# Performance work log

Measured on AMD Instinct MI355X. Metric: run time of the kernel, lower is better.

## Reference

```python
import jax, jax.numpy as jnp
import numpy as np

EMB = 128
N_TEXT = 80000
N_NODES = 100000
E = 800000
N_REL = 500
PRED_IN = 4 * EMB + 2 * 2 + 2 * 2 * (2 + 2)  # 532


def scatter_mean(x, src, dst, num_nodes):
    # PyG MessagePassing(aggr='mean'): mean of x[src] grouped by dst; empty groups -> 0
    sums = jax.ops.segment_sum(x[src], dst, num_segments=num_nodes)
    cnt = jax.ops.segment_sum(jnp.ones((src.shape[0], 1), x.dtype), dst, num_segments=num_nodes)
    return sums / jnp.maximum(cnt, 1.0)


def setup_inputs() -> dict:
    key = jax.random.key(0)
    ks = jax.random.split(key, 12)
    inp = {
        "h_id_tensor": jax.random.randint(ks[0], (E,), 0, N_NODES),
        "r_id_tensor": jax.random.randint(ks[1], (E,), 0, N_REL),
        "t_id_tensor": jax.random.randint(ks[2], (E,), 0, N_NODES),
        "q_emb": jax.random.normal(ks[3], (1, EMB), jnp.float32),
        "entity_embs": jax.random.normal(ks[4], (N_TEXT, EMB), jnp.float32),
        "num_non_text_entities": N_NODES - N_TEXT,
        "relation_embs": jax.random.normal(ks[5], (N_REL, EMB), jnp.float32),
        "topic_entity_one_hot": jax.random.uniform(ks[6], (N_NODES, 2), jnp.float32),
        # learned params
        "non_text_emb": jax.random.normal(ks[7], (1, EMB), jnp.float32) * 0.02,
        "W1": jax.random.normal(ks[8], (EMB, PRED_IN), jnp.float32) / np.sqrt(PRED_IN),
        "b1": jnp.zeros((EMB,), jnp.float32),
        "W2": jax.random.normal(ks[9], (1, EMB), jnp.float32) / np.sqrt(EMB),
        "b2": jnp.zeros((1,), jnp.float32),
    }
    return inp


def reference(h_id_tensor, r_id_tensor, t_id_tensor, q_emb, entity_embs,
              num_non_text_entities, relation_embs, topic_entity_one_hot,
              non_text_emb, W1, b1, W2, b2):
    num_nodes = entity_embs.shape[0] + num_non_text_entities
    # node embeddings: text entities + shared non-text embedding row
    h_e = jnp.concatenate(
        [entity_embs, jnp.broadcast_to(non_text_emb, (num_non_text_entities, EMB))], axis=0)

    # DDE: forward rounds over (h->t), reverse rounds over (t->h); scatter-mean diffusion
    dde_list = []
    h_pe = topic_entity_one_hot
    for _ in range(2):
        h_pe = scatter_mean(h_pe, h_id_tensor, t_id_tensor, num_nodes)
        dde_list.append(h_pe)
    h_pe_rev = topic_entity_one_hot
    for _ in range(2):
        h_pe_rev = scatter_mean(h_pe_rev, t_id_tensor, h_id_tensor, num_nodes)
        dde_list.append(h_pe_rev)

    h_e_full = jnp.concatenate([h_e, topic_entity_one_hot] + dde_list, axis=1)  # [N, EMB+10]

    h_r = relation_embs[r_id_tensor]                       # [E, EMB]
    h_q = jnp.broadcast_to(q_emb, (h_r.shape[0], EMB))     # [E, EMB]
    h_triple = jnp.concatenate(
        [h_q, h_e_full[h_id_tensor], h_r, h_e_full[t_id_tensor]], axis=1)  # [E, PRED_IN]

    hidden = jax.nn.relu(h_triple @ W1.T + b1)             # [E, EMB]
    pred = hidden @ W2.T + b2                              # [E, 1]
    return pred
```

## Files before the change

### kernel.cpp

```cpp
#include <hip/hip_runtime.h>

#define EMB 128
#define W1LD 532
#define KP 160
#define ST 264
#define BSH 8
#define BNODES 256
#define EPB 4096

typedef unsigned long long u64;
typedef unsigned int u32;
typedef unsigned short u16;
typedef __attribute__((ext_vector_type(8))) short short8;
typedef __attribute__((ext_vector_type(4))) float f32x4;
typedef _Float16 h2 __attribute__((ext_vector_type(2)));

__device__ __forceinline__ u16 f2bf(float x) {
    unsigned u = __float_as_uint(x);
    unsigned r = (u + 0x7fffu + ((u >> 16) & 1u)) >> 16;
    return (u16)r;
}
__device__ __forceinline__ u16 f2h(float x) {
    union { _Float16 h; u16 u; } c; c.h = (_Float16)x; return c.u;
}
__device__ __forceinline__ h2 u2h(unsigned u) {
    union { unsigned u; h2 h; } c; c.u = u; return c.h;
}

__device__ __forceinline__ float ep8(const uint4& ua, const uint4& ub,
                                     const uint4& ur, const uint4& uw, float s) {
    const h2 z = {(_Float16)0.0f, (_Float16)0.0f};
#if __has_builtin(__builtin_amdgcn_fdot2)
#define FDOT2(x, w, s) __builtin_amdgcn_fdot2(x, w, s, false)
#else
#define FDOT2(x, w, s) (s + (float)x[0] * (float)w[0] + (float)x[1] * (float)w[1])
#endif
#define EP1(c)                                                         \
    {                                                                  \
        h2 x = u2h(ua.c) + u2h(ur.c) + u2h(ub.c);                      \
        x = __builtin_elementwise_max(x, z);                           \
        h2 w = u2h(uw.c);                                              \
        s = FDOT2(x, w, s);                                            \
    }
    EP1(x) EP1(y) EP1(z) EP1(w)
#undef EP1
#undef FDOT2
    return s;
}

__global__ __launch_bounds__(1024) void khist(
    const int* __restrict__ h_id, const int* __restrict__ t_id,
    u32* __restrict__ hist, int E, int NBKT, int NSB)
{
    __shared__ u32 lh[1024];
    const int t = threadIdx.x, sb = blockIdx.x;
    const int rows = 2 * NBKT;
    for (int i = t; i < rows; i += 1024) lh[i] = 0;
    __syncthreads();
    const int base = sb * EPB;
#pragma unroll
    for (int c = 0; c < EPB / 1024; c++) {
        int e = base + c * 1024 + t;
        if (e < E) {
            atomicAdd(&lh[t_id[e] >> BSH], 1u);
            atomicAdd(&lh[NBKT + (h_id[e] >> BSH)], 1u);
        }
    }
    __syncthreads();
    for (int i = t; i < rows; i += 1024) hist[(size_t)i * NSB + sb] = lh[i];
}

__global__ __launch_bounds__(256) void kscanA(
    u32* __restrict__ hist, u32* __restrict__ tot, int NSB)
{
    __shared__ u32 s[256];
    const int t = threadIdx.x, row = blockIdx.x;
    u32 v = (t < NSB) ? hist[(size_t)row * NSB + t] : 0;
    s[t] = v;
    __syncthreads();
    for (int o = 1; o < 256; o <<= 1) {
        u32 x = (t >= o) ? s[t - o] : 0;
        __syncthreads();
        s[t] += x;
        __syncthreads();
    }
    if (t < NSB) hist[(size_t)row * NSB + t] = s[t] - v;
    if (t == 255) tot[row] = s[255];
}

__global__ __launch_bounds__(1024) void kbase(
    const u32* __restrict__ tot, u32* __restrict__ base,
    u32* __restrict__ bstart, int NBKT, int E)
{
    __shared__ u32 sc[1024];
    const int t = threadIdx.x;
    const int rows = 2 * NBKT;
    u32 v = (t < rows) ? tot[t] : 0;
    sc[t] = v;
    __syncthreads();
    for (int o = 1; o < 1024; o <<= 1) {
        u32 x = (t >= o) ? sc[t - o] : 0;
        __syncthreads();
        sc[t] += x;
        __syncthreads();
    }
    __syncthreads();
    if (t < rows) {
        u32 excl = sc[t] - v;
        u32 seg0 = (t >= NBKT) ? (sc[NBKT - 1 + 1 - 1] - 0) : 0;
        u32 segoff = (t >= NBKT) ? sc[NBKT - 1] : 0;
        (void)seg0;
        u32 b = excl - segoff;
        base[t] = b;
        const int seg = (t < NBKT) ? 0 : (NBKT + 1);
        const int b0  = (t < NBKT) ? 0 : NBKT;
        bstart[seg + (t - b0)] = b;
        if (t == b0) bstart[seg + NBKT] = (u32)E;
    }
}

__global__ __launch_bounds__(1024) void kplace(
    const int* __restrict__ h_id, const int* __restrict__ r_id,
    const int* __restrict__ t_id,
    const u32* __restrict__ hist, const u32* __restrict__ base,
    u32* __restrict__ perm_t, u64* __restrict__ perm_e,
    int E, int NBKT, int NSB)
{
    __shared__ u32 cur[1024];
    const int t = threadIdx.x, sb = blockIdx.x;
    const int rows = 2 * NBKT;
    if (t < rows) cur[t] = base[t] + hist[(size_t)t * NSB + sb];
    __syncthreads();
    const int ebase = sb * EPB;
#pragma unroll
    for (int c = 0; c < EPB / 1024; c++) {
        int e = ebase + c * 1024 + t;
        if (e < E) {
            int tt = t_id[e], h = h_id[e], r = r_id[e];
            u32 pt = atomicAdd(&cur[tt >> BSH], 1u);
            perm_t[pt] = (u32)h | ((u32)(tt & (BNODES - 1)) << 17);
            u32 ph = atomicAdd(&cur[NBKT + (h >> BSH)], 1u);
            perm_e[ph] = (u64)h | ((u64)tt << 17) | ((u64)r << 34)
                       | ((u64)e << 43);
        }
    }
}

__device__ __forceinline__ void scat_bucket(
    int d, int b, const u32* perm_t, const u64* perm_e, const u32* bstart,
    const float* srcv, float* out, int N, int NBKT, u64* acc)
{
    const int t = threadIdx.x;
    for (int i = t; i < BNODES; i += 256) acc[i] = 0;
    __syncthreads();
    const u32 s0 = bstart[d * (NBKT + 1) + b];
    const u32 s1 = bstart[d * (NBKT + 1) + b + 1];
    if (d == 0) {
        for (u32 i = s0 + t; i < s1; i += 256) {
            u32 rec  = perm_t[i];
            u32 src  = rec & 0x1FFFFu;
            u32 slot = rec >> 17;
            float2 v = *(const float2*)(srcv + 2 * src);
            u64 p = (u64)__float2uint_rn(v.x * 1048576.0f)
                  | ((u64)__float2uint_rn(v.y * 1048576.0f) << 26)
                  | (1ull << 52);
            atomicAdd(&acc[slot], p);
        }
    } else {
        for (u32 i = s0 + t; i < s1; i += 256) {
            u64 rec  = perm_e[i];
            u32 src  = (u32)(rec >> 17) & 0x1FFFFu;
            u32 slot = (u32)rec & (BNODES - 1);
            float2 v = *(const float2*)(srcv + 2 * src);
            u64 p = (u64)__float2uint_rn(v.x * 1048576.0f)
                  | ((u64)__float2uint_rn(v.y * 1048576.0f) << 26)
                  | (1ull << 52);
            atomicAdd(&acc[slot], p);
        }
    }
    __syncthreads();
    for (int i = t; i < BNODES; i += 256) {
        int node = b * BNODES + i;
        if (node < N) {
            u64 a = acc[i];
            float cnt = (float)(u32)(a >> 52);
            float inv = (1.0f / 1048576.0f) / fmaxf(cnt, 1.0f);
            float2 m;
            m.x = (float)(u32)(a & 0x3FFFFFFu) * inv;
            m.y = (float)(u32)((a >> 26) & 0x3FFFFFFu) * inv;
            *(float2*)(out + 2 * node) = m;
        }
    }
}

__device__ __forceinline__ void prep_block(
    int pb, const float* W1, const float* q, const float* rel,
    const float* b1, const float* W2,
    u16* WBF, float* qWb, u16* W2h, u16* Rbf, float* v )
{
    const int t = threadIdx.x;
    if (pb < KP) {
        int k = pb, n = t;
        float val = 0.0f;
        if (k < 138) {
            val = (n < 128) ? W1[(size_t)n * W1LD + 128 + k]
                            : W1[(size_t)(n - 128) * W1LD + 394 + k];
        }
        int kstep = k >> 5, quad = (k >> 3) & 3, j = k & 7;
        WBF[(((size_t)(kstep * 4 + quad) * 256 + n) << 3) + j] = f2bf(val);
        return;
    }
    int b = pb - KP;
    if (t < EMB) v[t] = (b == 0) ? q[t] : rel[(size_t)(b - 1) * EMB + t];
    __syncthreads();
    if (t < EMB) {
        const float* w = W1 + (size_t)t * W1LD + (b == 0 ? 0 : 266);
        float s = 0.0f;
#pragma unroll
        for (int k = 0; k < EMB; k += 4) {
            float4 wv = *(const float4*)(w + k);
            s += wv.x * v[k] + wv.y * v[k + 1] + wv.z * v[k + 2] + wv.w * v[k + 3];
        }
        if (b == 0) { qWb[t] = s + b1[t]; W2h[t] = f2h(W2[t]); }
        else        Rbf[(size_t)(b - 1) * EMB + t] = f2h(s);
    }
}

template<int ROUND>
__global__ __launch_bounds__(256) void kscat(
    const u32* __restrict__ perm_t, const u64* __restrict__ perm_e,
    const u32* __restrict__ bstart,
    const float* __restrict__ topic,
    const float* __restrict__ src_t, const float* __restrict__ src_h,
    float* __restrict__ out_t, float* __restrict__ out_h,
    const float* __restrict__ W1, const float* __restrict__ q,
    const float* __restrict__ rel, const float* __restrict__ b1,
    const float* __restrict__ W2,
    u16* __restrict__ WBF, float* __restrict__ qWb,
    u16* __restrict__ W2h, u16* __restrict__ Rbf,
    int N, int NBKT, int NREL)
{
    const int bid = blockIdx.x;
    if (bid < 2 * NBKT) {
        __shared__ u64 acc[BNODES];
        const int d = (bid < NBKT) ? 0 : 1;
        const float* srcv = (ROUND == 1) ? topic : (d ? src_h : src_t);
        scat_bucket(d, bid - d * NBKT, perm_t, perm_e, bstart,
                    srcv, d ? out_h : out_t, N, NBKT, acc);
        return;
    }
    if (ROUND != 1) return;
    __shared__ float v[EMB];
    prep_block(bid - 2 * NBKT, W1, q, rel, b1, W2, WBF, qWb, W2h, Rbf, v);
}

__global__ __launch_bounds__(256) void k2b_node(
    const float* __restrict__ ent, const float* __restrict__ nte,
    const float* __restrict__ topic,
    const float* __restrict__ dde1f, const float* __restrict__ dde2f,
    const float* __restrict__ dde3f, const float* __restrict__ dde4f,
    const u16* __restrict__ WBF, const float* __restrict__ qWb,
    u16* __restrict__ A, u16* __restrict__ B,
    int NT, int N)
{
    __shared__ __align__(16) u16 lds[32 * ST];
    const int t = threadIdx.x;
    const int lane = t & 63;
    const int w    = t >> 6;
    const int ln15 = lane & 15;
    const int quad = lane >> 4;
    const int m0   = (w & 1) * 16;
    const int n0   = (w >> 1) * 128;
    const int nblk = blockIdx.x * 32;

    {
        int m  = t >> 3;
        int kq = (t & 7) << 4;
        int gn = nblk + m;
        const float* src = (gn < N) ? ((gn < NT) ? ent + (size_t)gn * EMB + kq
                                                 : nte + kq)
                                    : nte;
        u16 pk[16];
#pragma unroll
        for (int p = 0; p < 4; p++) {
            float4 v = (gn < N) ? *(const float4*)(src + 4 * p)
                                : make_float4(0.f, 0.f, 0.f, 0.f);
            pk[4 * p + 0] = f2bf(v.x); pk[4 * p + 1] = f2bf(v.y);
            pk[4 * p + 2] = f2bf(v.z); pk[4 * p + 3] = f2bf(v.w);
        }
        *(uint4*)&lds[m * ST + kq]     = *(uint4*)&pk[0];
        *(uint4*)&lds[m * ST + kq + 8] = *(uint4*)&pk[8];
    }
    if (t < 32) {
        int gn = nblk + t;
        if (gn < N) {
            float2 tp = *(const float2*)(topic + 2 * gn);
            float2 d1 = *(const float2*)(dde1f + 2 * gn);
            float2 d2 = *(const float2*)(dde2f + 2 * gn);
            float2 d3 = *(const float2*)(dde3f + 2 * gn);
            float2 d4 = *(const float2*)(dde4f + 2 * gn);
            lds[t * ST + 128] = f2bf(tp.x); lds[t * ST + 129] = f2bf(tp.y);
            lds[t * ST + 130] = f2bf(d1.x); lds[t * ST + 131] = f2bf(d1.y);
            lds[t * ST + 132] = f2bf(d2.x); lds[t * ST + 133] = f2bf(d2.y);
            lds[t * ST + 134] = f2bf(d3.x); lds[t * ST + 135] = f2bf(d3.y);
            lds[t * ST + 136] = f2bf(d4.x); lds[t * ST + 137] = f2bf(d4.y);
        } else {
#pragma unroll
            for (int z = 128; z < 138; z++) lds[t * ST + z] = 0;
        }
#pragma unroll
        for (int z = 138; z < KP; z++) lds[t * ST + z] = 0;
    }
    __syncthreads();

    f32x4 acc[8];
#pragma unroll
    for (int i = 0; i < 8; i++) acc[i] = (f32x4){0.f, 0.f, 0.f, 0.f};

    const u16* wbbase = WBF + (((size_t)quad * 256 + n0 + ln15) << 3);
#pragma unroll
    for (int ks = 0; ks < 5; ks++) {
        short8 a = *(const short8*)&lds[(m0 + ln15) * ST + ks * 32 + quad * 8];
        const u16* wb = wbbase + ((size_t)ks * 4 * 256 * 8);
#pragma unroll
        for (int nt = 0; nt < 8; nt++) {
            short8 b = *(const short8*)(wb + (nt << 7));
            acc[nt] = __builtin_amdgcn_mfma_f32_16x16x32_bf16(a, b, acc[nt], 0, 0, 0);
        }
    }

    __syncthreads();
#pragma unroll
    for (int nt = 0; nt < 8; nt++) {
        int c = n0 + nt * 16 + ln15;
        float qv = (n0 == 0) ? qWb[c] : 0.0f;
#pragma unroll
        for (int r = 0; r < 4; r++) {
            int row = m0 + quad * 4 + r;
            lds[row * ST + c] = f2h(acc[nt][r] + qv);
        }
    }
    __syncthreads();
    {
        int m  = t >> 3;
        int c0 = (t & 7) * 32;
        int gn = nblk + m;
        if (gn < N) {
            uint4 v0 = *(uint4*)&lds[m * ST + c0];
            uint4 v1 = *(uint4*)&lds[m * ST + c0 + 8];
            uint4 v2 = *(uint4*)&lds[m * ST + c0 + 16];
            uint4 v3 = *(uint4*)&lds[m * ST + c0 + 24];
            u16* dst = (c0 < 128) ? (A + (size_t)gn * EMB + c0)
                                  : (B + (size_t)gn * EMB + (c0 - 128));
            ((uint4*)dst)[0] = v0;
            ((uint4*)dst)[1] = v1;
            ((uint4*)dst)[2] = v2;
            ((uint4*)dst)[3] = v3;
        }
    }
}

__global__ __launch_bounds__(256) void edge_pred_srt4(
    const u64* __restrict__ perm_e,
    const u16* __restrict__ A, const u16* __restrict__ B,
    const u16* __restrict__ Rbf, const u16* __restrict__ W2h,
    const float* __restrict__ b2, float* __restrict__ out, int E)
{
    const int t    = threadIdx.x;
    const int lane = t & 63;
    const int g    = lane >> 4;
    const int k    = lane & 15;
    const int wv   = t >> 6;
    const int i0   = (blockIdx.x * 16 + wv * 4 + g) * 4;

    const uint4 uw = *(const uint4*)(W2h + k * 8);
    const float bb = b2[0];

    u64 rec[4];
    bool val[4];
#pragma unroll
    for (int j = 0; j < 4; j++) {
        val[j] = (i0 + j) < E;
        rec[j] = val[j] ? perm_e[i0 + j] : 0;
    }
    uint4 ua[4], ub[4], ur[4];
#pragma unroll
    for (int j = 0; j < 4; j++) {
        u32 h  = (u32)rec[j] & 0x1FFFFu;
        u32 tt = (u32)(rec[j] >> 17) & 0x1FFFFu;
        u32 r  = (u32)(rec[j] >> 34) & 0x1FFu;
        ua[j] = *(const uint4*)(A + (size_t)h * EMB + k * 8);
        ub[j] = *(const uint4*)(B + (size_t)tt * EMB + k * 8);
        ur[j] = *(const uint4*)(Rbf + (size_t)r * EMB + k * 8);
    }
    float s[4];
#pragma unroll
    for (int j = 0; j < 4; j++) s[j] = ep8(ua[j], ub[j], ur[j], uw, 0.0f);
#pragma unroll
    for (int j = 0; j < 4; j++) {
        float v = s[j];
        v += __shfl_xor(v, 1, 64);
        v += __shfl_xor(v, 2, 64);
        v += __shfl_xor(v, 4, 64);
        v += __shfl_xor(v, 8, 64);
        if (k == 0 && val[j]) out[(u32)(rec[j] >> 43)] = v + bb;
    }
}

__global__ __launch_bounds__(256) void edge_pred_f16(
    const int* __restrict__ h_id, const int* __restrict__ r_id,
    const int* __restrict__ t_id,
    const u16* __restrict__ A, const u16* __restrict__ B,
    const u16* __restrict__ Rbf, const u16* __restrict__ W2h,
    const float* __restrict__ b2, float* __restrict__ out, int E)
{
    const int t    = threadIdx.x;
    const int lane = t & 63;
    const int g    = lane >> 4;
    const int k    = lane & 15;
    const int wv   = t >> 6;
    const int e    = blockIdx.x * 16 + wv * 4 + g;

    const uint4 uw = *(const uint4*)(W2h + k * 8);
    float s = 0.0f;
    if (e < E) {
        const int h = h_id[e], r = r_id[e], tt = t_id[e];
        const uint4 ua = *(const uint4*)(A + (size_t)h * EMB + k * 8);
        const uint4 ub = *(const uint4*)(B + (size_t)tt * EMB + k * 8);
        const uint4 ur = *(const uint4*)(Rbf + (size_t)r * EMB + k * 8);
        s = ep8(ua, ub, ur, uw, 0.0f);
    }
    s += __shfl_xor(s, 1, 64);
    s += __shfl_xor(s, 2, 64);
    s += __shfl_xor(s, 4, 64);
    s += __shfl_xor(s, 8, 64);
    if (k == 0 && e < E) out[e] = s + b2[0];
}


extern "C" void kernel_launch(void* const* d_in, const int* in_sizes, int n_in,
                              void* d_out, int out_size, void* d_ws, size_t ws_size,
                              hipStream_t stream)
{
    const int*   h_id  = (const int*)d_in[0];
    const int*   r_id  = (const int*)d_in[1];
    const int*   t_id  = (const int*)d_in[2];
    const float* q_emb = (const float*)d_in[3];
    const float* ent   = (const float*)d_in[4];
    const float* rel   = (const float*)d_in[6];
    const float* topic = (const float*)d_in[7];
    const float* nte   = (const float*)d_in[8];
    const float* W1    = (const float*)d_in[9];
    const float* b1    = (const float*)d_in[10];
    const float* W2    = (const float*)d_in[11];
    const float* b2    = (const float*)d_in[12];

    const int E    = in_sizes[0];
    const int NT   = in_sizes[4] / EMB;
    const int N    = in_sizes[7] / 2;
    const int NREL = in_sizes[6] / EMB;

    const int NBKT = (N + BNODES - 1) >> BSH;
    const int NSB  = (E + EPB - 1) / EPB;

    float* qWb  = (float*)d_ws;
    u16* W2h    = (u16*)(qWb + EMB);
    u16* Rbf    = W2h + EMB;
    u16* WBF    = Rbf + (size_t)NREL * EMB;
    float* dde1f = (float*)(WBF + (size_t)KP * 256);
    float* dde2f = dde1f + 2 * (size_t)N;
    float* dde3f = dde2f + 2 * (size_t)N;
    float* dde4f = dde3f + 2 * (size_t)N;
    u16* Aw = (u16*)(dde4f + 2 * (size_t)N);
    u16* Bw = Aw + (size_t)N * EMB;
    u64* perm_ded = (u64*)(Bw + (size_t)N * EMB);

    u32* hist   = (u32*)Aw;
    u32* tot    = hist + (size_t)2 * NBKT * NSB;
    u32* base   = tot + 2 * NBKT;
    u32* bstart = base + 2 * NBKT;
    u32* perm_t = bstart + 2 * (NBKT + 1);
    u64* perm_alias = (u64*)(((size_t)(perm_t + E) + 7) & ~(size_t)7);

    size_t need_srt = (size_t)((char*)(perm_ded + E) - (char*)d_ws);
    const bool srt = (ws_size >= need_srt) && (E < (1 << 20)) &&
                     (N <= (1 << 17)) && (NREL <= (1 << 9)) &&
                     (NSB <= 256) && (2 * NBKT <= 1024);
    u64* perm_e = srt ? perm_ded : perm_alias;

    const int nn = (N + 31) / 32;

    khist<<<NSB, 1024, 0, stream>>>(h_id, t_id, hist, E, NBKT, NSB);
    kscanA<<<2 * NBKT, 256, 0, stream>>>(hist, tot, NSB);
    kbase<<<1, 1024, 0, stream>>>(tot, base, bstart, NBKT, E);
    kplace<<<NSB, 1024, 0, stream>>>(h_id, r_id, t_id, hist, base,
                                     perm_t, perm_e, E, NBKT, NSB);

    kscat<1><<<2 * NBKT + KP + 1 + NREL, 256, 0, stream>>>(
        perm_t, perm_e, bstart, topic, nullptr, nullptr, dde1f, dde3f,
        W1, q_emb, rel, b1, W2, WBF, qWb, W2h, Rbf, N, NBKT, NREL);

    kscat<2><<<2 * NBKT, 256, 0, stream>>>(
        perm_t, perm_e, bstart, topic, dde1f, dde3f, dde2f, dde4f,
        W1, q_emb, rel, b1, W2, WBF, qWb, W2h, Rbf, N, NBKT, NREL);

    k2b_node<<<nn, 256, 0, stream>>>(
        ent, nte, topic, dde1f, dde2f, dde3f, dde4f,
        WBF, qWb, Aw, Bw, NT, N);

    if (srt) {
        edge_pred_srt4<<<(E + 63) / 64, 256, 0, stream>>>(
            perm_e, Aw, Bw, Rbf, W2h, b2, (float*)d_out, E);
    } else {
        edge_pred_f16<<<(E + 15) / 16, 256, 0, stream>>>(
            h_id, r_id, t_id, Aw, Bw, Rbf, W2h, b2, (float*)d_out, E);
    }
}
```

Before: 253.1 us.

## Fuse weight prep into histogram kernel, halve sort chunk, unroll scatter loads

Moves the W1/relation preprocessing blocks from the first scatter launch into the histogram launch, so they run alongside the histogram work instead of extending the first diffusion round. Halves the edges per sort block (more histogram/place blocks, 256-thread histogram blocks) and widens the per-row scan to 512 threads to match. Unrolls the scatter-mean loop by four so several gather loads are in flight before the LDS atomics. Risks include more hist rows to scan, extra kplace blocks, and higher register use in the scatter kernel.

Result: slower. 258.6 us (+2.2%).

```diff
diff --git a/kernel.cpp b/kernel.cpp
--- a/kernel.cpp
+++ b/kernel.cpp
@@ -6,7 +6,7 @@
 #define ST 264
 #define BSH 8
 #define BNODES 256
-#define EPB 4096
+#define EPB 2048
 
 typedef unsigned long long u64;
 typedef unsigned int u32;
@@ -25,6 +25,11 @@
 }
 __device__ __forceinline__ h2 u2h(unsigned u) {
     union { unsigned u; h2 h; } c; c.u = u; return c.h;
+}
+__device__ __forceinline__ u64 pk2(float2 v) {
+    return (u64)__float2uint_rn(v.x * 1048576.0f)
+         | ((u64)__float2uint_rn(v.y * 1048576.0f) << 26)
+         | (1ull << 52);
 }
 
 __device__ __forceinline__ float ep8(const uint4& ua, const uint4& ub,
@@ -48,44 +53,88 @@
     return s;
 }
 
-__global__ __launch_bounds__(1024) void khist(
+__device__ __forceinline__ void prep_block(
+    int pb, const float* W1, const float* q, const float* rel,
+    const float* b1, const float* W2,
+    u16* WBF, float* qWb, u16* W2h, u16* Rbf, float* v )
+{
+    const int t = threadIdx.x;
+    if (pb < KP) {
+        int k = pb, n = t;
+        float val = 0.0f;
+        if (k < 138) {
+            val = (n < 128) ? W1[(size_t)n * W1LD + 128 + k]
+                            : W1[(size_t)(n - 128) * W1LD + 394 + k];
+        }
+        int kstep = k >> 5, quad = (k >> 3) & 3, j = k & 7;
+        WBF[(((size_t)(kstep * 4 + quad) * 256 + n) << 3) + j] = f2bf(val);
+        return;
+    }
+    int b = pb - KP;
+    if (t < EMB) v[t] = (b == 0) ? q[t] : rel[(size_t)(b - 1) * EMB + t];
+    __syncthreads();
+    if (t < EMB) {
+        const float* w = W1 + (size_t)t * W1LD + (b == 0 ? 0 : 266);
+        float s = 0.0f;
+#pragma unroll
+        for (int k = 0; k < EMB; k += 4) {
+            float4 wv = *(const float4*)(w + k);
+            s += wv.x * v[k] + wv.y * v[k + 1] + wv.z * v[k + 2] + wv.w * v[k + 3];
+        }
+        if (b == 0) { qWb[t] = s + b1[t]; W2h[t] = f2h(W2[t]); }
+        else        Rbf[(size_t)(b - 1) * EMB + t] = f2h(s);
+    }
+}
+
+__global__ __launch_bounds__(256) void k_hist_prep(
     const int* __restrict__ h_id, const int* __restrict__ t_id,
-    u32* __restrict__ hist, int E, int NBKT, int NSB)
-{
-    __shared__ u32 lh[1024];
-    const int t = threadIdx.x, sb = blockIdx.x;
-    const int rows = 2 * NBKT;
-    for (int i = t; i < rows; i += 1024) lh[i] = 0;
-    __syncthreads();
-    const int base = sb * EPB;
-#pragma unroll
-    for (int c = 0; c < EPB / 1024; c++) {
-        int e = base + c * 1024 + t;
-        if (e < E) {
-            atomicAdd(&lh[t_id[e] >> BSH], 1u);
-            atomicAdd(&lh[NBKT + (h_id[e] >> BSH)], 1u);
-        }
-    }
-    __syncthreads();
-    for (int i = t; i < rows; i += 1024) hist[(size_t)i * NSB + sb] = lh[i];
-}
-
-__global__ __launch_bounds__(256) void kscanA(
+    u32* __restrict__ hist,
+    const float* __restrict__ W1, const float* __restrict__ q,
+    const float* __restrict__ rel, const float* __restrict__ b1,
+    const float* __restrict__ W2,
+    u16* __restrict__ WBF, float* __restrict__ qWb,
+    u16* __restrict__ W2h, u16* __restrict__ Rbf,
+    int E, int NBKT, int NSB, int NREL)
+{
+    const int bid = blockIdx.x, t = threadIdx.x;
+    if (bid < NSB) {
+        __shared__ u32 lh[1024];
+        const int rows = 2 * NBKT;
+        for (int i = t; i < rows; i += 256) lh[i] = 0;
+        __syncthreads();
+        const int base = bid * EPB;
+#pragma unroll
+        for (int c = 0; c < EPB / 256; c++) {
+            int e = base + c * 256 + t;
+            if (e < E) {
+                atomicAdd(&lh[t_id[e] >> BSH], 1u);
+                atomicAdd(&lh[NBKT + (h_id[e] >> BSH)], 1u);
+            }
+        }
+        __syncthreads();
+        for (int i = t; i < rows; i += 256) hist[(size_t)i * NSB + bid] = lh[i];
+        return;
+    }
+    __shared__ float v[EMB];
+    prep_block(bid - NSB, W1, q, rel, b1, W2, WBF, qWb, W2h, Rbf, v);
+}
+
+__global__ __launch_bounds__(512) void kscanA(
     u32* __restrict__ hist, u32* __restrict__ tot, int NSB)
 {
-    __shared__ u32 s[256];
+    __shared__ u32 s[512];
     const int t = threadIdx.x, row = blockIdx.x;
     u32 v = (t < NSB) ? hist[(size_t)row * NSB + t] : 0;
     s[t] = v;
     __syncthreads();
-    for (int o = 1; o < 256; o <<= 1) {
+    for (int o = 1; o < 512; o <<= 1) {
         u32 x = (t >= o) ? s[t - o] : 0;
         __syncthreads();
         s[t] += x;
         __syncthreads();
     }
     if (t < NSB) hist[(size_t)row * NSB + t] = s[t] - v;
-    if (t == 255) tot[row] = s[255];
+    if (t == 511) tot[row] = s[511];
 }
 
 __global__ __launch_bounds__(1024) void kbase(
@@ -107,9 +156,7 @@
     __syncthreads();
     if (t < rows) {
         u32 excl = sc[t] - v;
-        u32 seg0 = (t >= NBKT) ? (sc[NBKT - 1 + 1 - 1] - 0) : 0;
         u32 segoff = (t >= NBKT) ? sc[NBKT - 1] : 0;
-        (void)seg0;
         u32 b = excl - segoff;
         base[t] = b;
         const int seg = (t < NBKT) ? 0 : (NBKT + 1);
@@ -146,36 +193,61 @@
     }
 }
 
-__device__ __forceinline__ void scat_bucket(
-    int d, int b, const u32* perm_t, const u64* perm_e, const u32* bstart,
-    const float* srcv, float* out, int N, int NBKT, u64* acc)
-{
-    const int t = threadIdx.x;
+__global__ __launch_bounds__(256) void kscat(
+    const u32* __restrict__ perm_t, const u64* __restrict__ perm_e,
+    const u32* __restrict__ bstart,
+    const float* __restrict__ src_t, const float* __restrict__ src_h,
+    float* __restrict__ out_t, float* __restrict__ out_h,
+    int N, int NBKT)
+{
+    __shared__ u64 acc[BNODES];
+    const int bid = blockIdx.x, t = threadIdx.x;
+    const int d = (bid < NBKT) ? 0 : 1;
+    const int b = bid - d * NBKT;
+    const float* srcv = d ? src_h : src_t;
+    float* out = d ? out_h : out_t;
+
     for (int i = t; i < BNODES; i += 256) acc[i] = 0;
     __syncthreads();
     const u32 s0 = bstart[d * (NBKT + 1) + b];
     const u32 s1 = bstart[d * (NBKT + 1) + b + 1];
     if (d == 0) {
-        for (u32 i = s0 + t; i < s1; i += 256) {
-            u32 rec  = perm_t[i];
-            u32 src  = rec & 0x1FFFFu;
-            u32 slot = rec >> 17;
-            float2 v = *(const float2*)(srcv + 2 * src);
-            u64 p = (u64)__float2uint_rn(v.x * 1048576.0f)
-                  | ((u64)__float2uint_rn(v.y * 1048576.0f) << 26)
-                  | (1ull << 52);
-            atomicAdd(&acc[slot], p);
+        u32 i = s0 + t;
+        for (; i + 768 < s1; i += 1024) {
+            u32 r0 = perm_t[i], r1 = perm_t[i + 256];
+            u32 r2 = perm_t[i + 512], r3 = perm_t[i + 768];
+            float2 v0 = *(const float2*)(srcv + 2 * (r0 & 0x1FFFFu));
+            float2 v1 = *(const float2*)(srcv + 2 * (r1 & 0x1FFFFu));
+            float2 v2 = *(const float2*)(srcv + 2 * (r2 & 0x1FFFFu));
+            float2 v3 = *(const float2*)(srcv + 2 * (r3 & 0x1FFFFu));
+            atomicAdd(&acc[r0 >> 17], pk2(v0));
+            atomicAdd(&acc[r1 >> 17], pk2(v1));
+            atomicAdd(&acc[r2 >> 17], pk2(v2));
+            atomicAdd(&acc[r3 >> 17], pk2(v3));
+        }
+        for (; i < s1; i += 256) {
+            u32 rec = perm_t[i];
+            float2 v = *(const float2*)(srcv + 2 * (rec & 0x1FFFFu));
+            atomicAdd(&acc[rec >> 17], pk2(v));
         }
     } else {
-        for (u32 i = s0 + t; i < s1; i += 256) {
-            u64 rec  = perm_e[i];
-            u32 src  = (u32)(rec >> 17) & 0x1FFFFu;
-            u32 slot = (u32)rec & (BNODES - 1);
-            float2 v = *(const float2*)(srcv + 2 * src);
-            u64 p = (u64)__float2uint_rn(v.x * 1048576.0f)
-                  | ((u64)__float2uint_rn(v.y * 1048576.0f) << 26)
-                  | (1ull << 52);
-            atomicAdd(&acc[slot], p);
+        u32 i = s0 + t;
+        for (; i + 768 < s1; i += 1024) {
+            u64 r0 = perm_e[i], r1 = perm_e[i + 256];
+            u64 r2 = perm_e[i + 512], r3 = perm_e[i + 768];
+            float2 v0 = *(const float2*)(srcv + 2 * ((u32)(r0 >> 17) & 0x1FFFFu));
+            float2 v1 = *(const float2*)(srcv + 2 * ((u32)(r1 >> 17) & 0x1FFFFu));
+            float2 v2 = *(const float2*)(srcv + 2 * ((u32)(r2 >> 17) & 0x1FFFFu));
+            float2 v3 = *(const float2*)(srcv + 2 * ((u32)(r3 >> 17) & 0x1FFFFu));
+            atomicAdd(&acc[(u32)r0 & (BNODES - 1)], pk2(v0));
+            atomicAdd(&acc[(u32)r1 & (BNODES - 1)], pk2(v1));
+            atomicAdd(&acc[(u32)r2 & (BNODES - 1)], pk2(v2));
+            atomicAdd(&acc[(u32)r3 & (BNODES - 1)], pk2(v3));
+        }
+        for (; i < s1; i += 256) {
+            u64 rec = perm_e[i];
+            float2 v = *(const float2*)(srcv + 2 * ((u32)(rec >> 17) & 0x1FFFFu));
+            atomicAdd(&acc[(u32)rec & (BNODES - 1)], pk2(v));
         }
     }
     __syncthreads();
@@ -191,67 +263,6 @@
             *(float2*)(out + 2 * node) = m;
         }
     }
-}
-
-__device__ __forceinline__ void prep_block(
-    int pb, const float* W1, const float* q, const float* rel,
-    const float* b1, const float* W2,
-    u16* WBF, float* qWb, u16* W2h, u16* Rbf, float* v )
-{
-    const int t = threadIdx.x;
-    if (pb < KP) {
-        int k = pb, n = t;
-        float val = 0.0f;
-        if (k < 138) {
-            val = (n < 128) ? W1[(size_t)n * W1LD + 128 + k]
-                            : W1[(size_t)(n - 128) * W1LD + 394 + k];
-        }
-        int kstep = k >> 5, quad = (k >> 3) & 3, j = k & 7;
-        WBF[(((size_t)(kstep * 4 + quad) * 256 + n) << 3) + j] = f2bf(val);
-        return;
-    }
-    int b = pb - KP;
-    if (t < EMB) v[t] = (b == 0) ? q[t] : rel[(size_t)(b - 1) * EMB + t];
-    __syncthreads();
-    if (t < EMB) {
-        const float* w = W1 + (size_t)t * W1LD + (b == 0 ? 0 : 266);
-        float s = 0.0f;
-#pragma unroll
-        for (int k = 0; k < EMB; k += 4) {
-            float4 wv = *(const float4*)(w + k);
-            s += wv.x * v[k] + wv.y * v[k + 1] + wv.z * v[k + 2] + wv.w * v[k + 3];
-        }
-        if (b == 0) { qWb[t] = s + b1[t]; W2h[t] = f2h(W2[t]); }
-        else        Rbf[(size_t)(b - 1) * EMB + t] = f2h(s);
-    }
-}
-
-template<int ROUND>
-__global__ __launch_bounds__(256) void kscat(
-    const u32* __restrict__ perm_t, const u64* __restrict__ perm_e,
-    const u32* __restrict__ bstart,
-    const float* __restrict__ topic,
-    const float* __restrict__ src_t, const float* __restrict__ src_h,
-    float* __restrict__ out_t, float* __restrict__ out_h,
-    const float* __restrict__ W1, const float* __restrict__ q,
-    const float* __restrict__ rel, const float* __restrict__ b1,
-    const float* __restrict__ W2,
-    u16* __restrict__ WBF, float* __restrict__ qWb,
-    u16* __restrict__ W2h, u16* __restrict__ Rbf,
-    int N, int NBKT, int NREL)
-{
-    const int bid = blockIdx.x;
-    if (bid < 2 * NBKT) {
-        __shared__ u64 acc[BNODES];
-        const int d = (bid < NBKT) ? 0 : 1;
-        const float* srcv = (ROUND == 1) ? topic : (d ? src_h : src_t);
-        scat_bucket(d, bid - d * NBKT, perm_t, perm_e, bstart,
-                    srcv, d ? out_h : out_t, N, NBKT, acc);
-        return;
-    }
-    if (ROUND != 1) return;
-    __shared__ float v[EMB];
-    prep_block(bid - 2 * NBKT, W1, q, rel, b1, W2, WBF, qWb, W2h, Rbf, v);
 }
 
 __global__ __launch_bounds__(256) void k2b_node(
@@ -485,24 +496,25 @@
     size_t need_srt = (size_t)((char*)(perm_ded + E) - (char*)d_ws);
     const bool srt = (ws_size >= need_srt) && (E < (1 << 20)) &&
                      (N <= (1 << 17)) && (NREL <= (1 << 9)) &&
-                     (NSB <= 256) && (2 * NBKT <= 1024);
+                     (NSB <= 512) && (2 * NBKT <= 1024);
     u64* perm_e = srt ? perm_ded : perm_alias;
 
     const int nn = (N + 31) / 32;
 
-    khist<<<NSB, 1024, 0, stream>>>(h_id, t_id, hist, E, NBKT, NSB);
-    kscanA<<<2 * NBKT, 256, 0, stream>>>(hist, tot, NSB);
+    k_hist_prep<<<NSB + KP + 1 + NREL, 256, 0, stream>>>(
+        h_id, t_id, hist, W1, q_emb, rel, b1, W2,
+        WBF, qWb, W2h, Rbf, E, NBKT, NSB, NREL);
+
+    kscanA<<<2 * NBKT, 512, 0, stream>>>(hist, tot, NSB);
     kbase<<<1, 1024, 0, stream>>>(tot, base, bstart, NBKT, E);
+
     kplace<<<NSB, 1024, 0, stream>>>(h_id, r_id, t_id, hist, base,
                                      perm_t, perm_e, E, NBKT, NSB);
 
-    kscat<1><<<2 * NBKT + KP + 1 + NREL, 256, 0, stream>>>(
-        perm_t, perm_e, bstart, topic, nullptr, nullptr, dde1f, dde3f,
-        W1, q_emb, rel, b1, W2, WBF, qWb, W2h, Rbf, N, NBKT, NREL);
-
-    kscat<2><<<2 * NBKT, 256, 0, stream>>>(
-        perm_t, perm_e, bstart, topic, dde1f, dde3f, dde2f, dde4f,
-        W1, q_emb, rel, b1, W2, WBF, qWb, W2h, Rbf, N, NBKT, NREL);
+    kscat<<<2 * NBKT, 256, 0, stream>>>(
+        perm_t, perm_e, bstart, topic, topic, dde1f, dde3f, N, NBKT);
+    kscat<<<2 * NBKT, 256, 0, stream>>>(
+        perm_t, perm_e, bstart, dde1f, dde3f, dde2f, dde4f, N, NBKT);
 
     k2b_node<<<nn, 256, 0, stream>>>(
         ent, nte, topic, dde1f, dde2f, dde3f, dde4f,
```

## Double bucket and chunk sizes and fold bucket-base scan into placement kernel

Applied to the files above, without the earlier changes.

Doubles the bucket width (512 nodes per bucket) and edges per sort block, halving the number of buckets and sort blocks. The single-block kbase scan kernel is removed: each kplace block now redundantly scans the bucket totals itself, and block 0 writes the bucket start table. This removes one kernel launch and its serialization, at the cost of redundant scan work per block, fewer and larger buckets for the downstream scatter kernels, and a new fallback condition requiring 2*NBKT <= 512.

Result: no change. 256.9 us (+1.5%).

```diff
diff --git a/kernel.cpp b/kernel.cpp
--- a/kernel.cpp
+++ b/kernel.cpp
@@ -4,9 +4,9 @@
 #define W1LD 532
 #define KP 160
 #define ST 264
-#define BSH 8
-#define BNODES 256
-#define EPB 4096
+#define BSH 9
+#define BNODES 512
+#define EPB 8192
 
 typedef unsigned long long u64;
 typedef unsigned int u32;
@@ -52,10 +52,10 @@
     const int* __restrict__ h_id, const int* __restrict__ t_id,
     u32* __restrict__ hist, int E, int NBKT, int NSB)
 {
-    __shared__ u32 lh[1024];
+    __shared__ u32 lh[512];
     const int t = threadIdx.x, sb = blockIdx.x;
     const int rows = 2 * NBKT;
-    for (int i = t; i < rows; i += 1024) lh[i] = 0;
+    if (t < rows) lh[t] = 0;
     __syncthreads();
     const int base = sb * EPB;
 #pragma unroll
@@ -67,7 +67,7 @@
         }
     }
     __syncthreads();
-    for (int i = t; i < rows; i += 1024) hist[(size_t)i * NSB + sb] = lh[i];
+    if (t < rows) hist[(size_t)t * NSB + sb] = lh[t];
 }
 
 __global__ __launch_bounds__(256) void kscanA(
@@ -88,12 +88,17 @@
     if (t == 255) tot[row] = s[255];
 }
 
-__global__ __launch_bounds__(1024) void kbase(
-    const u32* __restrict__ tot, u32* __restrict__ base,
-    u32* __restrict__ bstart, int NBKT, int E)
+__global__ __launch_bounds__(1024) void kplace(
+    const int* __restrict__ h_id, const int* __restrict__ r_id,
+    const int* __restrict__ t_id,
+    const u32* __restrict__ hist, const u32* __restrict__ tot,
+    u32* __restrict__ bstart,
+    u32* __restrict__ perm_t, u64* __restrict__ perm_e,
+    int E, int NBKT, int NSB)
 {
     __shared__ u32 sc[1024];
-    const int t = threadIdx.x;
+    __shared__ u32 cur[512];
+    const int t = threadIdx.x, sb = blockIdx.x;
     const int rows = 2 * NBKT;
     u32 v = (t < rows) ? tot[t] : 0;
     sc[t] = v;
@@ -104,32 +109,18 @@
         sc[t] += x;
         __syncthreads();
     }
-    __syncthreads();
     if (t < rows) {
         u32 excl = sc[t] - v;
-        u32 seg0 = (t >= NBKT) ? (sc[NBKT - 1 + 1 - 1] - 0) : 0;
         u32 segoff = (t >= NBKT) ? sc[NBKT - 1] : 0;
-        (void)seg0;
-        u32 b = excl - segoff;
-        base[t] = b;
-        const int seg = (t < NBKT) ? 0 : (NBKT + 1);
-        const int b0  = (t < NBKT) ? 0 : NBKT;
-        bstart[seg + (t - b0)] = b;
-        if (t == b0) bstart[seg + NBKT] = (u32)E;
-    }
-}
-
-__global__ __launch_bounds__(1024) void kplace(
-    const int* __restrict__ h_id, const int* __restrict__ r_id,
-    const int* __restrict__ t_id,
-    const u32* __restrict__ hist, const u32* __restrict__ base,
-    u32* __restrict__ perm_t, u64* __restrict__ perm_e,
-    int E, int NBKT, int NSB)
-{
-    __shared__ u32 cur[1024];
-    const int t = threadIdx.x, sb = blockIdx.x;
-    const int rows = 2 * NBKT;
-    if (t < rows) cur[t] = base[t] + hist[(size_t)t * NSB + sb];
+        u32 base = excl - segoff;
+        cur[t] = base + hist[(size_t)t * NSB + sb];
+        if (sb == 0) {
+            const int seg = (t < NBKT) ? 0 : (NBKT + 1);
+            const int b0  = (t < NBKT) ? 0 : NBKT;
+            bstart[seg + (t - b0)] = base;
+            if (t == b0) bstart[seg + NBKT] = (u32)E;
+        }
+    }
     __syncthreads();
     const int ebase = sb * EPB;
 #pragma unroll
@@ -477,23 +468,21 @@
 
     u32* hist   = (u32*)Aw;
     u32* tot    = hist + (size_t)2 * NBKT * NSB;
-    u32* base   = tot + 2 * NBKT;
-    u32* bstart = base + 2 * NBKT;
+    u32* bstart = tot + 2 * NBKT;
     u32* perm_t = bstart + 2 * (NBKT + 1);
     u64* perm_alias = (u64*)(((size_t)(perm_t + E) + 7) & ~(size_t)7);
 
     size_t need_srt = (size_t)((char*)(perm_ded + E) - (char*)d_ws);
     const bool srt = (ws_size >= need_srt) && (E < (1 << 20)) &&
                      (N <= (1 << 17)) && (NREL <= (1 << 9)) &&
-                     (NSB <= 256) && (2 * NBKT <= 1024);
+                     (NSB <= 256) && (2 * NBKT <= 512);
     u64* perm_e = srt ? perm_ded : perm_alias;
 
     const int nn = (N + 31) / 32;
 
     khist<<<NSB, 1024, 0, stream>>>(h_id, t_id, hist, E, NBKT, NSB);
     kscanA<<<2 * NBKT, 256, 0, stream>>>(hist, tot, NSB);
-    kbase<<<1, 1024, 0, stream>>>(tot, base, bstart, NBKT, E);
-    kplace<<<NSB, 1024, 0, stream>>>(h_id, r_id, t_id, hist, base,
+    kplace<<<NSB, 1024, 0, stream>>>(h_id, r_id, t_id, hist, tot, bstart,
                                      perm_t, perm_e, E, NBKT, NSB);
 
     kscat<1><<<2 * NBKT + KP + 1 + NREL, 256, 0, stream>>>(
```
